# Performance work log

Hardware: AMD Instinct MI355X
Metric: run time of the kernel (lower is better)

Reference implementation:

```python
import jax, jax.numpy as jnp
import numpy as np
from jax.scipy.special import gammaln

# Problem sizes (static)
N = 50000          # nodes
P = 200000         # paths (source->target pairs in the transitive closure)
L = 6              # edges (nodes) per path -> flat edge list length E = P*L
E = P * L
MAX_DELAY = 128
DT = 1.0
T = int(MAX_DELAY * int(1 / DT))   # expanded time window (== 128)
EPS = 1e-12


def gamma_irf(params):
    """IRF_FN entry: per-node gamma (Nash-cascade) impulse response, [N, T]."""
    a = jax.nn.softplus(params[:, 0]) + 1.0      # shape  > 1
    b = jax.nn.softplus(params[:, 1]) + 0.5      # scale  > 0.5
    t = (jnp.arange(T, dtype=jnp.float32) + 0.5) * jnp.float32(DT)  # [T]
    log_irf = ((a[:, None] - 1.0) * jnp.log(t)[None, :]
               - t[None, :] / b[:, None]
               - gammaln(a)[:, None]
               - a[:, None] * jnp.log(b)[:, None])
    return jnp.exp(log_irf) * jnp.float32(DT)    # [N, T]


def setup_inputs() -> dict:
    key = jax.random.key(0)
    k1, k2 = jax.random.split(key)
    params = jax.random.normal(k1, (N, 2), dtype=jnp.float32)
    edges_flat = jax.random.randint(k2, (E,), 0, N, dtype=jnp.int32)
    path_cumsum = jnp.arange(P + 1, dtype=jnp.int32) * L  # segment offsets into edges_flat
    return {"params": params, "edges_flat": edges_flat, "path_cumsum": path_cumsum}


def reference(params, edges_flat, path_cumsum):
    # --- irf_fn + rfft ---------------------------------------------------
    irfs = gamma_irf(params)                          # [N, T]
    irfs_freq = jnp.fft.rfft(irfs, n=T, axis=-1)      # [N, F] complex64

    # --- log_transitive_closure: product of per-edge spectra along paths -
    log_f = jnp.log(irfs_freq + EPS)                  # complex log, [N, F]
    seg_ids = jnp.searchsorted(path_cumsum[1:], jnp.arange(E, dtype=path_cumsum.dtype),
                               side="right")          # [E] path id per flat edge
    path_log = jax.ops.segment_sum(log_f[edges_flat], seg_ids, num_segments=P)  # [P, F]
    path_freq = jnp.exp(path_log)                     # product along path, [P, F]

    # coords: (source node, target node) of each path; include_index_diag appends (i, i)
    src = edges_flat[path_cumsum[:-1]]
    dst = edges_flat[path_cumsum[1:] - 1]
    diag = jnp.arange(N, dtype=edges_flat.dtype)
    coords = jnp.stack([jnp.concatenate([src, diag]),
                        jnp.concatenate([dst, diag])])              # [2, P+N]
    freq_all = jnp.concatenate([path_freq, irfs_freq], axis=0)      # [P+N, F]

    # --- irfft + postprocessing ------------------------------------------
    irfs_agg = jnp.fft.irfft(freq_all, n=T, axis=-1)  # [P+N, T]
    irfs_agg = jax.nn.relu(irfs_agg)
    # sampler.phi_k: avg-pool by factor int(1/dt) == 1 -> identity when dt=1
    irfs_agg = jnp.flip(irfs_agg, axis=-1)
    irfs_agg = irfs_agg / (jnp.sum(irfs_agg, axis=-1, keepdims=True) + EPS)
    # SparseKernel(coords, values, kernel_size=(N, N, T)) -> return its contents
    return (coords, irfs_agg)
```

## Files before the change

### kernel.cpp

```cpp
#include <hip/hip_runtime.h>
#include <hip/hip_bf16.h>

#define N_NODES 50000
#define P_PATHS 200000
#define N_ROWS  250000
#define L_EDGES 6
#define T_LEN   128
#define F_BINS  65
#define EPSF    1e-12f
#define PIF     3.14159265358979323846f
#define COORD_ELEMS ((size_t)2 * (P_PATHS + N_NODES))
#define FREQ_BYTES  ((size_t)N_NODES * F_BINS * 8)
#define KDIM  128
#define KPADN 128
#define ROWS_BLK 64

typedef _Float16 v2h __attribute__((ext_vector_type(2)));
typedef _Float16 v8h __attribute__((ext_vector_type(8)));
typedef float    v4f __attribute__((ext_vector_type(4)));

__device__ __forceinline__ int swzA(int row, int h) {
    return (((h >> 3) ^ (row & 7)) << 3) | (h & 7);
}

__device__ __forceinline__ float softplus_(float x) {
    const float e = __expf(-fabsf(x));
    return fmaxf(x, 0.0f) + __logf(1.0f + e);
}

__device__ __forceinline__ float lgamma_pos_(float x) {
    const float ser = 1.000000000190015f
                    + 76.18009172947146f     / (x + 1.0f)
                    - 86.50532032941677f     / (x + 2.0f)
                    + 24.01409824083091f     / (x + 3.0f)
                    - 1.231739572450155f     / (x + 4.0f)
                    + 0.1208650973866179e-2f / (x + 5.0f)
                    - 0.5395239384953e-5f    / (x + 6.0f);
    const float tmp = x + 5.5f;
    return (x + 0.5f) * __logf(tmp) - tmp + __logf(2.5066282746310005f * ser / x);
}

__global__ void irfa49s_wgen(_Float16* __restrict__ Wt) {
    const int idx = blockIdx.x * 256 + threadIdx.x;
    if (idx >= 128 * KDIM) return;
    const int t  = idx / KDIM;
    const int kk = idx - t * KDIM;
    int j; float cj; bool is_sin;
    if (kk == 1) { j = 64; cj = 1.0f; is_sin = false; }
    else {
        j = kk >> 1;
        cj = (j == 0) ? 1.0f : 2.0f;
        is_sin = (kk & 1);
    }
    const int m = (j * t) & 127;
    const float th = (float)m * (PIF / 64.0f);
    const float tri = is_sin ? -__sinf(th) : __cosf(th);
    Wt[idx] = (_Float16)(cj * tri * (1.0f / 128.0f));
}

__global__ void irfa49s_freq(const float* __restrict__ params, _Float16* __restrict__ freqh) {
    __shared__ float sx[8][T_LEN];
    __shared__ float su[8][64];
    __shared__ float sv[8][64];
    const int tid  = threadIdx.x;
    const int slot = tid >> 5;
    const int tl   = tid & 31;
    const int n    = blockIdx.x * 8 + slot;
    _Float16* fh   = freqh + (size_t)n * KPADN;

    const float a  = softplus_(params[2 * n + 0]) + 1.0f;
    const float b  = softplus_(params[2 * n + 1]) + 0.5f;
    const float lg = lgamma_pos_(a);
    const float lb = __logf(b);
    const float rb = 1.0f / b;
    const float am1 = a - 1.0f;
    const float cst = -lg - a * lb;

    float S = 0.0f;
    #pragma unroll
    for (int j = 0; j < 4; ++j) {
        const float tc = (float)(tl + 32 * j) + 0.5f;
        const float x  = __expf(fmaf(am1, __logf(tc), fmaf(-tc, rb, cst)));
        sx[slot][tl + 32 * j] = x;
        S += x;
    }

    float s0  = S;
    float s64 = (tl & 1) ? -S : S;
    float c32 = ((tl & 3) == 0) ? S : (((tl & 3) == 2) ? -S : 0.0f);
    float s32 = ((tl & 3) == 1) ? S : (((tl & 3) == 3) ? -S : 0.0f);
    #pragma unroll
    for (int m = 16; m; m >>= 1) {
        s0  += __shfl_xor(s0, m);
        s64 += __shfl_xor(s64, m);
        c32 += __shfl_xor(c32, m);
        s32 += __shfl_xor(s32, m);
    }
    __syncthreads();

    {
        const int i1 = tl + 1;
        const float xa = sx[slot][i1], xb = sx[slot][T_LEN - i1];
        su[slot][i1] = xa + xb;
        sv[slot][i1] = xa - xb;
        if (tl < 31) {
            const int i2 = tl + 33;
            const float xc = sx[slot][i2], xd = sx[slot][T_LEN - i2];
            su[slot][i2] = xc + xd;
            sv[slot][i2] = xc - xd;
        }
    }
    __syncthreads();

    if (tl == 0) {
        v2h h;
        h[0] = (_Float16)s0;  h[1] = (_Float16)s64;   *(v2h*)(fh + 0)  = h;
        h[0] = (_Float16)c32; h[1] = (_Float16)(-s32); *(v2h*)(fh + 64) = h;
        return;
    }

    const float x0v  = sx[slot][0];
    const float x64v = sx[slot][64];
    const int   k    = tl;
    const float th   = (float)k * (PIF / 64.0f);
    const float c1 = __cosf(th), s1 = __sinf(th);
    const float c2 = 2.0f * c1 * c1 - 1.0f;
    const float s2 = 2.0f * s1 * c1;
    const float K  = 2.0f * c2;

    float ue1 = 0.0f, ue2 = 0.0f, ve1 = 0.0f, ve2 = 0.0f;
    float uo1 = 0.0f, uo2 = 0.0f, vo1 = 0.0f, vo2 = 0.0f;
    #pragma unroll
    for (int m = 31; m >= 1; --m) {
        const float2 uu = *(const float2*)&su[slot][2 * m];
        const float2 vv = *(const float2*)&sv[slot][2 * m];
        float v0;
        v0 = fmaf(K, ue1, uu.x - ue2); ue2 = ue1; ue1 = v0;
        v0 = fmaf(K, ve1, vv.x - ve2); ve2 = ve1; ve1 = v0;
        v0 = fmaf(K, uo1, uu.y - uo2); uo2 = uo1; uo1 = v0;
        v0 = fmaf(K, vo1, vv.y - vo2); vo2 = vo1; vo1 = v0;
    }
    {
        float v0;
        v0 = fmaf(K, uo1, su[slot][1] - uo2); uo2 = uo1; uo1 = v0;
        v0 = fmaf(K, vo1, sv[slot][1] - vo2); vo2 = vo1; vo1 = v0;
    }

    const float Ec = fmaf(ue1, c2, -ue2);
    const float Es = ve1 * s2;
    const float ReSu = fmaf(-uo2, c2, uo1);
    const float ImSu = uo2 * s2;
    const float Oc   = c1 * ReSu - s1 * ImSu;
    const float ReSv = fmaf(-vo2, c2, vo1);
    const float ImSv = vo2 * s2;
    const float Os   = s1 * ReSv + c1 * ImSv;

    const float base = x0v + ((k & 1) ? -x64v : x64v);
    v2h h;
    h[0] = (_Float16)(base + Ec + Oc);
    h[1] = (_Float16)(-(Es + Os));
    *(v2h*)(fh + 2 * k) = h;
    h[0] = (_Float16)(base + Ec - Oc);
    h[1] = (_Float16)(Es - Os);
    *(v2h*)(fh + 2 * (64 - k)) = h;
}

__global__ __launch_bounds__(256) void irfa49s_paths(const _Float16* __restrict__ freqh,
                                                     const int* __restrict__ edges,
                                                     const _Float16* __restrict__ Wt,
                                                     float* __restrict__ out_agg) {
    __shared__ _Float16 sA[ROWS_BLK * KDIM];
    const int tid   = threadIdx.x;
    const int rbase = blockIdx.x * ROWS_BLK;
    const int slot  = tid >> 5;
    const int tl    = tid & 31;

    #pragma unroll
    for (int pass = 0; pass < 8; ++pass) {
        const int rho = pass * 8 + slot;
        const int r   = rbase + rho;
        _Float16* rowp = sA + rho * KDIM;
        if (r < P_PATHS) {
            const int eb = r * L_EDGES;
            v2h av[L_EDGES], bv[L_EDGES];
            #pragma unroll
            for (int j = 0; j < L_EDGES; ++j) {
                const _Float16* fh = freqh + (size_t)edges[eb + j] * KPADN;
                av[j] = *(const v2h*)(fh + 2 * tl);
                bv[j] = *(const v2h*)(fh + 64 + 2 * tl);
            }
            float p1r = 1.0f, p1i = 0.0f, p2r = 1.0f, p2i = 0.0f, q = 1.0f;
            #pragma unroll
            for (int j = 0; j < L_EDGES; ++j) {
                const float ax  = (float)av[j][0];
                const float ayr = (float)av[j][1];
                const float ay  = (tl == 0) ? 0.0f : ayr;
                float t1 = p1r * ax - p1i * ay;
                p1i      = p1r * ay + p1i * ax;
                p1r = t1;
                q *= ayr;
                const float bx = (float)bv[j][0], by = (float)bv[j][1];
                float t2 = p2r * bx - p2i * by;
                p2i      = p2r * by + p2i * bx;
                p2r = t2;
            }
            v2h h;
            h[0] = (_Float16)p1r;
            h[1] = (tl == 0) ? (_Float16)q : (_Float16)p1i;
            *(v2h*)&rowp[swzA(rho, 2 * tl)] = h;
            h[0] = (_Float16)p2r; h[1] = (_Float16)p2i;
            *(v2h*)&rowp[swzA(rho, 64 + 2 * tl)] = h;
        } else {
            v2h av = (v2h){(_Float16)0.0f, (_Float16)0.0f};
            v2h bv = av;
            if (r < N_ROWS) {
                const _Float16* fh = freqh + (size_t)(r - P_PATHS) * KPADN;
                av = *(const v2h*)(fh + 2 * tl);
                bv = *(const v2h*)(fh + 64 + 2 * tl);
            }
            *(v2h*)&rowp[swzA(rho, 2 * tl)] = av;
            *(v2h*)&rowp[swzA(rho, 64 + 2 * tl)] = bv;
        }
    }
    __syncthreads();

    const int wv    = tid >> 6;
    const int lane  = tid & 63;
    const int arow  = wv * 16 + (lane & 15);
    const int kgrp  = (lane >> 4) * 8;
    const int tcol  = lane & 15;

    v4f acc[8];
    #pragma unroll
    for (int nt = 0; nt < 8; ++nt) acc[nt] = (v4f){0.0f, 0.0f, 0.0f, 0.0f};

    #pragma unroll
    for (int kt = 0; kt < 4; ++kt) {
        const int kk = kt * 32 + kgrp;
        const v8h afrag = *(const v8h*)&sA[arow * KDIM + swzA(arow, kk)];
        #pragma unroll
        for (int nt = 0; nt < 8; ++nt) {
            const int t = nt * 16 + tcol;
            const v8h bfrag = *(const v8h*)&Wt[t * KDIM + kk];
            acc[nt] = __builtin_amdgcn_mfma_f32_16x16x32_f16(afrag, bfrag, acc[nt], 0, 0, 0);
        }
    }

    const int rgrp = (lane >> 4) * 4;
    #pragma unroll
    for (int reg = 0; reg < 4; ++reg) {
        float vals[8];
        float vsum = 0.0f;
        #pragma unroll
        for (int nt = 0; nt < 8; ++nt) {
            const float v = fmaxf(acc[nt][reg], 0.0f);
            vals[nt] = v;
            vsum += v;
        }
        vsum += __shfl_xor(vsum, 1);
        vsum += __shfl_xor(vsum, 2);
        vsum += __shfl_xor(vsum, 4);
        vsum += __shfl_xor(vsum, 8);
        const int row = rbase + wv * 16 + rgrp + reg;
        if (row < N_ROWS) {
            const float inv = 1.0f / (vsum + EPSF);
            float* op = out_agg + (size_t)row * T_LEN;
            #pragma unroll
            for (int nt = 0; nt < 8; ++nt) {
                const int t = nt * 16 + tcol;
                op[127 - t] = vals[nt] * inv;
            }
        }
    }
}

__global__ void IRFAggregator_39049842655549_kernel(const int* __restrict__ edges,
                                                    float* __restrict__ out) {
    const int M = P_PATHS + N_NODES;
    const int i = blockIdx.x * blockDim.x + threadIdx.x;
    if (i >= 2 * M) return;
    int v;
    if (i < P_PATHS) {
        v = edges[i * L_EDGES];
    } else if (i < M) {
        v = i - P_PATHS;
    } else {
        const int j = i - M;
        if (j < P_PATHS) v = edges[j * L_EDGES + L_EDGES - 1];
        else             v = j - P_PATHS;
    }
    out[i] = (float)v;
}

extern "C" void kernel_launch(void* const* d_in, const int* in_sizes, int n_in,
                              void* d_out, int out_size, void* d_ws, size_t ws_size,
                              hipStream_t stream) {
    const float* params = (const float*)d_in[0];
    const int*   edges  = (const int*)d_in[1];

    _Float16* freqh = (_Float16*)d_ws;
    _Float16* Wt    = (_Float16*)((char*)d_ws + FREQ_BYTES);
    float* out      = (float*)d_out;
    float* out_agg  = out + COORD_ELEMS;

    IRFAggregator_39049842655549_kernel<<<(int)((COORD_ELEMS + 255) / 256), 256, 0, stream>>>(edges, out);
    irfa49s_wgen<<<(128 * KDIM + 255) / 256, 256, 0, stream>>>(Wt);
    irfa49s_freq<<<N_NODES / 8, 256, 0, stream>>>(params, freqh);
    irfa49s_paths<<<(N_ROWS + ROWS_BLK - 1) / ROWS_BLK, 256, 0, stream>>>(freqh, edges, Wt, out_agg);
}
```

Baseline: 137.6 us.

## Split path spectral product and GEMM into separate kernels via global staging buffer

The fused paths kernel is split in two. The first computes each path's frequency-domain product, or copies the diagonal node spectra, into a global fp16 staging tile. The second loads that tile into shared memory and runs the MFMA inverse-DFT GEMM. This separates the latency-bound gather from the matrix-core work so each kernel can get its own occupancy and scheduling, at the cost of an extra 64 MB global write and read plus one more launch.

After: 153.6 us. 11.6% more time.

```diff
diff --git a/kernel.cpp b/kernel.cpp
--- a/kernel.cpp
+++ b/kernel.cpp
@@ -11,6 +11,7 @@
 #define PIF     3.14159265358979323846f
 #define COORD_ELEMS ((size_t)2 * (P_PATHS + N_NODES))
 #define FREQ_BYTES  ((size_t)N_NODES * F_BINS * 8)
+#define ATILE_OFF   ((size_t)32 * 1024 * 1024)
 #define KDIM  128
 #define KPADN 128
 #define ROWS_BLK 64
@@ -114,7 +115,7 @@
 
     if (tl == 0) {
         v2h h;
-        h[0] = (_Float16)s0;  h[1] = (_Float16)s64;   *(v2h*)(fh + 0)  = h;
+        h[0] = (_Float16)s0;  h[1] = (_Float16)s64;    *(v2h*)(fh + 0)  = h;
         h[0] = (_Float16)c32; h[1] = (_Float16)(-s32); *(v2h*)(fh + 64) = h;
         return;
     }
@@ -165,61 +166,69 @@
     *(v2h*)(fh + 2 * (64 - k)) = h;
 }
 
-__global__ __launch_bounds__(256) void irfa49s_paths(const _Float16* __restrict__ freqh,
-                                                     const int* __restrict__ edges,
-                                                     const _Float16* __restrict__ Wt,
-                                                     float* __restrict__ out_agg) {
+__global__ __launch_bounds__(256) void irfa49t_prod(const _Float16* __restrict__ freqh,
+                                                    const int* __restrict__ edges,
+                                                    _Float16* __restrict__ Atile) {
+    const int gt  = blockIdx.x * 256 + threadIdx.x;
+    const int row = gt >> 5;
+    const int tl  = gt & 31;
+    _Float16* op = Atile + (size_t)row * KDIM;
+
+    if (row < P_PATHS) {
+        const int eb = row * L_EDGES;
+        v2h av[L_EDGES], bv[L_EDGES];
+        #pragma unroll
+        for (int j = 0; j < L_EDGES; ++j) {
+            const _Float16* fh = freqh + (size_t)edges[eb + j] * KPADN;
+            av[j] = *(const v2h*)(fh + 2 * tl);
+            bv[j] = *(const v2h*)(fh + 64 + 2 * tl);
+        }
+        float p1r = 1.0f, p1i = 0.0f, p2r = 1.0f, p2i = 0.0f, q = 1.0f;
+        #pragma unroll
+        for (int j = 0; j < L_EDGES; ++j) {
+            const float ax  = (float)av[j][0];
+            const float ayr = (float)av[j][1];
+            const float ay  = (tl == 0) ? 0.0f : ayr;
+            float t1 = p1r * ax - p1i * ay;
+            p1i      = p1r * ay + p1i * ax;
+            p1r = t1;
+            q *= ayr;
+            const float bx = (float)bv[j][0], by = (float)bv[j][1];
+            float t2 = p2r * bx - p2i * by;
+            p2i      = p2r * by + p2i * bx;
+            p2r = t2;
+        }
+        v2h h;
+        h[0] = (_Float16)p1r;
+        h[1] = (tl == 0) ? (_Float16)q : (_Float16)p1i;
+        *(v2h*)(op + 2 * tl) = h;
+        h[0] = (_Float16)p2r; h[1] = (_Float16)p2i;
+        *(v2h*)(op + 64 + 2 * tl) = h;
+    } else {
+        const _Float16* fh = freqh + (size_t)(row - P_PATHS) * KPADN;
+        *(v2h*)(op + 2 * tl)      = *(const v2h*)(fh + 2 * tl);
+        *(v2h*)(op + 64 + 2 * tl) = *(const v2h*)(fh + 64 + 2 * tl);
+    }
+}
+
+__global__ __launch_bounds__(256) void irfa49t_gemm(const _Float16* __restrict__ Atile,
+                                                    const _Float16* __restrict__ Wt,
+                                                    float* __restrict__ out_agg) {
     __shared__ _Float16 sA[ROWS_BLK * KDIM];
     const int tid   = threadIdx.x;
     const int rbase = blockIdx.x * ROWS_BLK;
-    const int slot  = tid >> 5;
-    const int tl    = tid & 31;
-
-    #pragma unroll
-    for (int pass = 0; pass < 8; ++pass) {
-        const int rho = pass * 8 + slot;
-        const int r   = rbase + rho;
-        _Float16* rowp = sA + rho * KDIM;
-        if (r < P_PATHS) {
-            const int eb = r * L_EDGES;
-            v2h av[L_EDGES], bv[L_EDGES];
-            #pragma unroll
-            for (int j = 0; j < L_EDGES; ++j) {
-                const _Float16* fh = freqh + (size_t)edges[eb + j] * KPADN;
-                av[j] = *(const v2h*)(fh + 2 * tl);
-                bv[j] = *(const v2h*)(fh + 64 + 2 * tl);
-            }
-            float p1r = 1.0f, p1i = 0.0f, p2r = 1.0f, p2i = 0.0f, q = 1.0f;
-            #pragma unroll
-            for (int j = 0; j < L_EDGES; ++j) {
-                const float ax  = (float)av[j][0];
-                const float ayr = (float)av[j][1];
-                const float ay  = (tl == 0) ? 0.0f : ayr;
-                float t1 = p1r * ax - p1i * ay;
-                p1i      = p1r * ay + p1i * ax;
-                p1r = t1;
-                q *= ayr;
-                const float bx = (float)bv[j][0], by = (float)bv[j][1];
-                float t2 = p2r * bx - p2i * by;
-                p2i      = p2r * by + p2i * bx;
-                p2r = t2;
-            }
-            v2h h;
-            h[0] = (_Float16)p1r;
-            h[1] = (tl == 0) ? (_Float16)q : (_Float16)p1i;
-            *(v2h*)&rowp[swzA(rho, 2 * tl)] = h;
-            h[0] = (_Float16)p2r; h[1] = (_Float16)p2i;
-            *(v2h*)&rowp[swzA(rho, 64 + 2 * tl)] = h;
-        } else {
-            v2h av = (v2h){(_Float16)0.0f, (_Float16)0.0f};
-            v2h bv = av;
-            if (r < N_ROWS) {
-                const _Float16* fh = freqh + (size_t)(r - P_PATHS) * KPADN;
-                av = *(const v2h*)(fh + 2 * tl);
-                bv = *(const v2h*)(fh + 64 + 2 * tl);
-            }
-            *(v2h*)&rowp[swzA(rho, 2 * tl)] = av;
-            *(v2h*)&rowp[swzA(rho, 64 + 2 * tl)] = bv;
+
+    {
+        const int rho = tid >> 2;
+        const int c0  = (tid & 3) * 32;
+        const int row = rbase + rho;
+        #pragma unroll
+        for (int c = 0; c < 4; ++c) {
+            const int h = c0 + c * 8;
+            v8h v = (v8h){(_Float16)0.0f, (_Float16)0.0f, (_Float16)0.0f, (_Float16)0.0f,
+                          (_Float16)0.0f, (_Float16)0.0f, (_Float16)0.0f, (_Float16)0.0f};
+            if (row < N_ROWS) v = *(const v8h*)&Atile[(size_t)row * KDIM + h];
+            *(v8h*)&sA[rho * KDIM + swzA(rho, h)] = v;
         }
     }
     __syncthreads();
@@ -300,11 +309,13 @@
 
     _Float16* freqh = (_Float16*)d_ws;
     _Float16* Wt    = (_Float16*)((char*)d_ws + FREQ_BYTES);
+    _Float16* Atile = (_Float16*)((char*)d_ws + ATILE_OFF);
     float* out      = (float*)d_out;
     float* out_agg  = out + COORD_ELEMS;
 
     IRFAggregator_39049842655549_kernel<<<(int)((COORD_ELEMS + 255) / 256), 256, 0, stream>>>(edges, out);
     irfa49s_wgen<<<(128 * KDIM + 255) / 256, 256, 0, stream>>>(Wt);
     irfa49s_freq<<<N_NODES / 8, 256, 0, stream>>>(params, freqh);
-    irfa49s_paths<<<(N_ROWS + ROWS_BLK - 1) / ROWS_BLK, 256, 0, stream>>>(freqh, edges, Wt, out_agg);
-}
+    irfa49t_prod<<<(N_ROWS * 32) / 256, 256, 0, stream>>>(freqh, edges, Atile);
+    irfa49t_gemm<<<(N_ROWS + ROWS_BLK - 1) / ROWS_BLK, 256, 0, stream>>>(Atile, Wt, out_agg);
+}
```
